# Optimization experiments

Hardware: AMD Instinct MI355X
Metric: run time of the kernel (lower is better)

Reference implementation:

```python
import jax, jax.numpy as jnp
import numpy as np

B, T = 16, 8192                       # batch, padded tokens per image
NUM_BINS, IN_CH = 4, 3
TOKEN_DIM = NUM_BINS ** 2 * (IN_CH + 2)   # 'interpolate', drop_delta=False -> 80
EMB_DIM = 384


def setup_inputs() -> dict:
    key = jax.random.key(0)
    k1, k2, k3, k4 = jax.random.split(key, 4)
    feat = jax.random.normal(k1, (B * T, TOKEN_DIM), dtype=jnp.float32)
    amask = jax.random.randint(k2, (B, T), 0, 2).astype(bool)
    amask = amask.at[:, 0].set(True)               # cls slot always valid
    g_idx = (jnp.arange(B, dtype=jnp.int32) * T)   # row index of cls token per image
    b_idx = jnp.repeat(jnp.arange(B, dtype=jnp.int32), T)
    W = jax.random.normal(k3, (EMB_DIM, TOKEN_DIM), dtype=jnp.float32) / np.sqrt(TOKEN_DIM).astype(np.float32)
    bias = jax.random.normal(k4, (EMB_DIM,), dtype=jnp.float32) * 0.001  # bias.data.mul_(0.001)
    cls_token = jnp.full((EMB_DIM,), 1e-5, dtype=jnp.float32)            # zeros + 1e-5
    return dict(feat=feat, amask=amask, g_idx=g_idx, b_idx=b_idx,
                W=W, bias=bias, cls_token=cls_token)


def reference(feat, amask, g_idx, b_idx, W, bias, cls_token):
    # MaskedLinear: gather masked rows -> linear -> scatter into zeros.
    # Equivalent dense form: compute y everywhere, zero out unmasked rows
    # (identity activation, so f(x)@W = masked-gather result exactly).
    mask = amask.reshape(-1)                                 # [B*T]
    y = feat @ W.T + bias                                    # [B*T, EMB_DIM]
    out = jnp.where(mask[:, None], y, jnp.zeros((), y.dtype))
    # cls-token insert: feat[g_idx] = cls_token (expanded over batch)
    out = out.at[g_idx].set(jnp.broadcast_to(cls_token, (g_idx.shape[0], EMB_DIM)))
    return out, amask, g_idx, b_idx
```

## Files before the change

kernel.cpp:

```cpp
#include <hip/hip_runtime.h>
#include <hip/hip_bf16.h>

#define TK 80
#define TN 384
#define BM 64

typedef __attribute__((ext_vector_type(8)))  __bf16 bf16x8;
typedef __attribute__((ext_vector_type(16))) float  f32x16;

__device__ __forceinline__ unsigned short f2bf_bits(float f) {
    unsigned int u = __float_as_uint(f);
    return (unsigned short)((u + 0x7fffu + ((u >> 16) & 1u)) >> 16);
}

union BF8 { unsigned short u[8]; bf16x8 v; };

__device__ __forceinline__ bf16x8 pack8(float4 f0, float4 f1) {
    BF8 r;
    r.u[0] = f2bf_bits(f0.x); r.u[1] = f2bf_bits(f0.y);
    r.u[2] = f2bf_bits(f0.z); r.u[3] = f2bf_bits(f0.w);
    r.u[4] = f2bf_bits(f1.x); r.u[5] = f2bf_bits(f1.y);
    r.u[6] = f2bf_bits(f1.z); r.u[7] = f2bf_bits(f1.w);
    return r.v;
}

__global__ __launch_bounds__(256) void tok_prep(
    const unsigned char* __restrict__ amask,
    const int* __restrict__ gidx,
    const int* __restrict__ bidx,
    float* __restrict__ out_amask,
    float* __restrict__ out_gidx,
    float* __restrict__ out_bidx,
    int BT, int B)
{
    const unsigned int* w32 = (const unsigned int*)amask;
    unsigned int w = w32[threadIdx.x & 255];
    int bytemode = __syncthreads_or((int)((w & 0xFFFFFF00u) != 0u));

    int i = blockIdx.x * blockDim.x + threadIdx.x;
    if (i < BT) {
        float m;
        if (bytemode) m = (float)amask[i];
        else          m = (float)(w32[i] & 1u);
        out_amask[i] = m;
        out_bidx[i]  = (float)bidx[i];
        if (i < B) out_gidx[i] = (float)gidx[i];
    }
}

__global__ __launch_bounds__(256) void tok_gemm_mfma(
    const float* __restrict__ feat,
    const float* __restrict__ W,
    const float* __restrict__ bias,
    const float* __restrict__ cls,
    const float* __restrict__ maskf,
    float* __restrict__ out,
    int T)
{
    const int lane   = threadIdx.x & 63;
    const int wave   = threadIdx.x >> 6;
    const int row0   = blockIdx.x * BM;
    const int colb   = wave * 96;
    const int lrow   = lane & 31;
    const int khalf  = lane >> 5;

    bf16x8 bfrag[3][5];
    #pragma unroll
    for (int nt = 0; nt < 3; ++nt) {
        const float* wrow = W + (size_t)(colb + nt * 32 + lrow) * TK;
        #pragma unroll
        for (int ks = 0; ks < 5; ++ks) {
            const float* p = wrow + ks * 16 + khalf * 8;
            float4 f0 = *(const float4*)p;
            float4 f1 = *(const float4*)(p + 4);
            bfrag[nt][ks] = pack8(f0, f1);
        }
    }

    float mv = maskf[row0 + lane];

    float bv[3], cv[3];
    #pragma unroll
    for (int nt = 0; nt < 3; ++nt) {
        int c = colb + nt * 32 + lrow;
        bv[nt] = bias[c];
        cv[nt] = cls[c];
    }

    f32x16 acc[2][3];
    #pragma unroll
    for (int mt = 0; mt < 2; ++mt)
        #pragma unroll
        for (int nt = 0; nt < 3; ++nt)
            acc[mt][nt] = (f32x16)0.0f;

    #pragma unroll
    for (int ks = 0; ks < 5; ++ks) {
        #pragma unroll
        for (int mt = 0; mt < 2; ++mt) {
            const float* frow = feat + (size_t)(row0 + mt * 32 + lrow) * TK
                              + ks * 16 + khalf * 8;
            float4 f0 = *(const float4*)frow;
            float4 f1 = *(const float4*)(frow + 4);
            bf16x8 a = pack8(f0, f1);
            #pragma unroll
            for (int nt = 0; nt < 3; ++nt)
                acc[mt][nt] = __builtin_amdgcn_mfma_f32_32x32x16_bf16(
                    a, bfrag[nt][ks], acc[mt][nt], 0, 0, 0);
        }
    }

    #pragma unroll
    for (int mt = 0; mt < 2; ++mt) {
        #pragma unroll
        for (int reg = 0; reg < 16; ++reg) {
            int rlocal = mt * 32 + 4 * khalf + (reg & 3) + 8 * (reg >> 2);
            float m = __shfl(mv, rlocal);
            int row = row0 + rlocal;
            bool iscls = (row % T) == 0;
            #pragma unroll
            for (int nt = 0; nt < 3; ++nt) {
                float v = m * (acc[mt][nt][reg] + bv[nt]);
                if (iscls) v = cv[nt];
                out[(size_t)row * TN + colb + nt * 32 + lrow] = v;
            }
        }
    }
}

extern "C" void kernel_launch(void* const* d_in, const int* in_sizes, int n_in,
                              void* d_out, int out_size, void* d_ws, size_t ws_size,
                              hipStream_t stream) {
    const float*         feat  = (const float*)d_in[0];
    const unsigned char* amask = (const unsigned char*)d_in[1];
    const int*           gidx  = (const int*)d_in[2];
    const int*           bidx  = (const int*)d_in[3];
    const float*         W     = (const float*)d_in[4];
    const float*         bias  = (const float*)d_in[5];
    const float*         cls   = (const float*)d_in[6];

    const int BT = in_sizes[1];
    const int B  = in_sizes[2];
    const int T  = BT / B;

    float* out       = (float*)d_out;
    float* out_amask = out + (size_t)BT * TN;
    float* out_gidx  = out_amask + BT;
    float* out_bidx  = out_gidx + B;

    tok_prep<<<(BT + 255) / 256, 256, 0, stream>>>(
        amask, gidx, bidx, out_amask, out_gidx, out_bidx, BT, B);

    tok_gemm_mfma<<<BT / BM, 256, 0, stream>>>(
        feat, W, bias, cls, out_amask, out, T);
}
```

Measured before the change: 58.37 us.

## Fuse mask prep into GEMM kernel and swap MFMA operands for row-contiguous float4 stores

Merges the separate mask/index conversion kernel into the MFMA GEMM kernel, so one launch and the round trip through the float mask buffer go away. The MFMA operand order is swapped (W as A, feat as B), which transposes the accumulator layout so each lane holds four consecutive output columns of a single row and can write float4 stores. Feature loads are hoisted ahead of the weight conversion so more memory requests are in flight. The cost is more live registers from staging all feature floats at once, which may reduce occupancy.

Measured after the change: 78.67 us. 34.8% more time.

```diff
diff --git a/kernel.cpp b/kernel.cpp
--- a/kernel.cpp
+++ b/kernel.cpp
@@ -1,5 +1,4 @@
 #include <hip/hip_runtime.h>
-#include <hip/hip_bf16.h>
 
 #define TK 80
 #define TN 384
@@ -24,68 +23,74 @@
     return r.v;
 }
 
-__global__ __launch_bounds__(256) void tok_prep(
+__global__ __launch_bounds__(256) void tok_fused(
+    const float* __restrict__ feat,
     const unsigned char* __restrict__ amask,
     const int* __restrict__ gidx,
     const int* __restrict__ bidx,
+    const float* __restrict__ W,
+    const float* __restrict__ bias,
+    const float* __restrict__ cls,
+    float* __restrict__ out,
     float* __restrict__ out_amask,
     float* __restrict__ out_gidx,
     float* __restrict__ out_bidx,
-    int BT, int B)
+    int B, int T)
 {
+    const int tid   = threadIdx.x;
+    const int lane  = tid & 63;
+    const int wave  = tid >> 6;
+    const int row0  = blockIdx.x * BM;
+    const int colb  = wave * 96;
+    const int lrow  = lane & 31;
+    const int khalf = lane >> 5;
+
     const unsigned int* w32 = (const unsigned int*)amask;
-    unsigned int w = w32[threadIdx.x & 255];
-    int bytemode = __syncthreads_or((int)((w & 0xFFFFFF00u) != 0u));
+    unsigned int wprobe = w32[tid & 255];
+    int bytemode = __syncthreads_or((int)((wprobe & 0xFFFFFF00u) != 0u));
 
-    int i = blockIdx.x * blockDim.x + threadIdx.x;
-    if (i < BT) {
-        float m;
-        if (bytemode) m = (float)amask[i];
-        else          m = (float)(w32[i] & 1u);
-        out_amask[i] = m;
-        out_bidx[i]  = (float)bidx[i];
-        if (i < B) out_gidx[i] = (float)gidx[i];
+    if (tid < BM) {
+        int r = row0 + tid;
+        out_amask[r] = bytemode ? (float)amask[r] : (float)(w32[r] & 1u);
+        out_bidx[r]  = (float)bidx[r];
     }
-}
+    if (blockIdx.x == 0 && tid < B) out_gidx[tid] = (float)gidx[tid];
 
-__global__ __launch_bounds__(256) void tok_gemm_mfma(
-    const float* __restrict__ feat,
-    const float* __restrict__ W,
-    const float* __restrict__ bias,
-    const float* __restrict__ cls,
-    const float* __restrict__ maskf,
-    float* __restrict__ out,
-    int T)
-{
-    const int lane   = threadIdx.x & 63;
-    const int wave   = threadIdx.x >> 6;
-    const int row0   = blockIdx.x * BM;
-    const int colb   = wave * 96;
-    const int lrow   = lane & 31;
-    const int khalf  = lane >> 5;
+    float mymask[2];
+    #pragma unroll
+    for (int mt = 0; mt < 2; ++mt) {
+        int r = row0 + mt * 32 + lrow;
+        mymask[mt] = bytemode ? (float)amask[r] : (float)(w32[r] & 1u);
+    }
 
-    bf16x8 bfrag[3][5];
+    float4 ff0[5][2], ff1[5][2];
+    #pragma unroll
+    for (int ks = 0; ks < 5; ++ks)
+        #pragma unroll
+        for (int mt = 0; mt < 2; ++mt) {
+            const float* p = feat + (size_t)(row0 + mt * 32 + lrow) * TK
+                           + ks * 16 + khalf * 8;
+            ff0[ks][mt] = *(const float4*)p;
+            ff1[ks][mt] = *(const float4*)(p + 4);
+        }
+
+    bf16x8 wfrag[3][5];
     #pragma unroll
     for (int nt = 0; nt < 3; ++nt) {
         const float* wrow = W + (size_t)(colb + nt * 32 + lrow) * TK;
         #pragma unroll
         for (int ks = 0; ks < 5; ++ks) {
             const float* p = wrow + ks * 16 + khalf * 8;
-            float4 f0 = *(const float4*)p;
-            float4 f1 = *(const float4*)(p + 4);
-            bfrag[nt][ks] = pack8(f0, f1);
+            wfrag[nt][ks] = pack8(*(const float4*)p, *(const float4*)(p + 4));
         }
     }
 
-    float mv = maskf[row0 + lane];
-
-    float bv[3], cv[3];
+    bf16x8 ffrag[5][2];
     #pragma unroll
-    for (int nt = 0; nt < 3; ++nt) {
-        int c = colb + nt * 32 + lrow;
-        bv[nt] = bias[c];
-        cv[nt] = cls[c];
-    }
+    for (int ks = 0; ks < 5; ++ks)
+        #pragma unroll
+        for (int mt = 0; mt < 2; ++mt)
+            ffrag[ks][mt] = pack8(ff0[ks][mt], ff1[ks][mt]);
 
     f32x16 acc[2][3];
     #pragma unroll
@@ -95,34 +100,39 @@
             acc[mt][nt] = (f32x16)0.0f;
 
     #pragma unroll
-    for (int ks = 0; ks < 5; ++ks) {
+    for (int ks = 0; ks < 5; ++ks)
         #pragma unroll
-        for (int mt = 0; mt < 2; ++mt) {
-            const float* frow = feat + (size_t)(row0 + mt * 32 + lrow) * TK
-                              + ks * 16 + khalf * 8;
-            float4 f0 = *(const float4*)frow;
-            float4 f1 = *(const float4*)(frow + 4);
-            bf16x8 a = pack8(f0, f1);
+        for (int mt = 0; mt < 2; ++mt)
             #pragma unroll
             for (int nt = 0; nt < 3; ++nt)
                 acc[mt][nt] = __builtin_amdgcn_mfma_f32_32x32x16_bf16(
-                    a, bfrag[nt][ks], acc[mt][nt], 0, 0, 0);
-        }
-    }
+                    wfrag[nt][ks], ffrag[ks][mt], acc[mt][nt], 0, 0, 0);
+
+    float4 bv[3][4];
+    #pragma unroll
+    for (int nt = 0; nt < 3; ++nt)
+        #pragma unroll
+        for (int q = 0; q < 4; ++q)
+            bv[nt][q] = *(const float4*)(bias + colb + nt * 32 + 8 * q + 4 * khalf);
 
     #pragma unroll
     for (int mt = 0; mt < 2; ++mt) {
+        const int row = row0 + mt * 32 + lrow;
+        const float m = mymask[mt];
+        const bool iscls = (row % T) == 0;
+        float* orow = out + (size_t)row * TN;
         #pragma unroll
-        for (int reg = 0; reg < 16; ++reg) {
-            int rlocal = mt * 32 + 4 * khalf + (reg & 3) + 8 * (reg >> 2);
-            float m = __shfl(mv, rlocal);
-            int row = row0 + rlocal;
-            bool iscls = (row % T) == 0;
+        for (int nt = 0; nt < 3; ++nt) {
             #pragma unroll
-            for (int nt = 0; nt < 3; ++nt) {
-                float v = m * (acc[mt][nt][reg] + bv[nt]);
-                if (iscls) v = cv[nt];
-                out[(size_t)row * TN + colb + nt * 32 + lrow] = v;
+            for (int q = 0; q < 4; ++q) {
+                const int col = colb + nt * 32 + 8 * q + 4 * khalf;
+                float4 v;
+                v.x = m * (acc[mt][nt][4 * q + 0] + bv[nt][q].x);
+                v.y = m * (acc[mt][nt][4 * q + 1] + bv[nt][q].y);
+                v.z = m * (acc[mt][nt][4 * q + 2] + bv[nt][q].z);
+                v.w = m * (acc[mt][nt][4 * q + 3] + bv[nt][q].w);
+                if (iscls) v = *(const float4*)(cls + col);
+                *(float4*)(orow + col) = v;
             }
         }
     }
@@ -148,9 +158,7 @@
     float* out_gidx  = out_amask + BT;
     float* out_bidx  = out_gidx + B;
 
-    tok_prep<<<(BT + 255) / 256, 256, 0, stream>>>(
-        amask, gidx, bidx, out_amask, out_gidx, out_bidx, BT, B);
-
-    tok_gemm_mfma<<<BT / BM, 256, 0, stream>>>(
-        feat, W, bias, cls, out_amask, out, T);
+    tok_fused<<<BT / BM, 256, 0, stream>>>(
+        feat, amask, gidx, bidx, W, bias, cls,
+        out, out_amask, out_gidx, out_bidx, B, T);
 }
```
